# Kernel tuning notes

Measured on AMD Instinct MI355X. Metric: run time of the kernel, lower is better.

## Reference

```python
import jax, jax.numpy as jnp
import numpy as np

B, T, N, F, C, H, O = 4, 8, 4096, 32, 32, 64, 1
RADIUS = 50.0   # adjacency_threshold on pairwise distance
EPS = 1e-5      # batchnorm eps


def setup_inputs() -> dict:
    key = jax.random.key(0)
    ks = jax.random.split(key, 8)
    x = jax.random.normal(ks[0], (B, T, N, F), jnp.float32)
    # dist_mat from random 2D node locations in a 1000x1000 area; avg degree ~32
    loc = jax.random.uniform(ks[1], (N, 2), jnp.float32) * 1000.0
    d2 = jnp.sum((loc[:, None, :] - loc[None, :, :]) ** 2, axis=-1)  # [N,N]
    adj = (d2 < RADIUS ** 2).astype(jnp.float32)                     # includes self (d=0)
    dinv = 1.0 / jnp.sqrt(jnp.maximum(adj.sum(-1), 1.0))
    adj_norm = adj * dinv[:, None] * dinv[None, :]                   # D^-1/2 A D^-1/2
    s = 0.05
    return dict(
        x=x,
        adj_norm=adj_norm,
        bn_gamma=jnp.ones((F,), jnp.float32),
        bn_beta=jnp.zeros((F,), jnp.float32),
        W_gcn=jax.random.normal(ks[2], (F, C), jnp.float32) * s,
        b_gcn=jnp.zeros((C,), jnp.float32),
        W_ih=jax.random.normal(ks[3], (C, 3 * H), jnp.float32) * s,
        W_hh=jax.random.normal(ks[4], (H, 3 * H), jnp.float32) * s,
        b_ih=jnp.zeros((3 * H,), jnp.float32),
        b_hh=jnp.zeros((3 * H,), jnp.float32),
        W_dense=jax.random.normal(ks[5], (H, O), jnp.float32) * s,
        b_dense=jnp.zeros((O,), jnp.float32),
    )


def reference(x, adj_norm, bn_gamma, bn_beta, W_gcn, b_gcn, W_ih, W_hh, b_ih, b_hh, W_dense, b_dense):
    # BatchNorm2d over feature channel (training-mode batch stats, biased var)
    mean = x.mean(axis=(0, 1, 2))
    var = x.var(axis=(0, 1, 2))
    xn = (x - mean) * jax.lax.rsqrt(var + EPS) * bn_gamma + bn_beta  # [B,T,N,F]
    # GCN association (same math every timestep -> batch over T)
    ya = jnp.einsum('mn,btnf->btmf', adj_norm, xn)                   # neighbor aggregate
    y = jnp.einsum('btnf,fc->btnc', ya, W_gcn) + b_gcn               # [B,T,N,C]
    # precompute input-gate projections, then scan GRU cell over time
    gi = jnp.einsum('btnc,ch->btnh', y, W_ih) + b_ih                 # [B,T,N,3H]
    gi = jnp.transpose(gi, (1, 0, 2, 3))                             # [T,B,N,3H]

    def step(h, g):
        gh = h @ W_hh + b_hh
        r = jax.nn.sigmoid(g[..., :H] + gh[..., :H])
        z = jax.nn.sigmoid(g[..., H:2 * H] + gh[..., H:2 * H])
        n = jnp.tanh(g[..., 2 * H:] + r * gh[..., 2 * H:])
        h_new = (1.0 - z) * n + z * h
        return h_new, h_new

    h0 = jnp.zeros((B, N, H), x.dtype)
    _, hs = jax.lax.scan(step, h0, gi)                               # [T,B,N,H]
    out = jnp.transpose(hs, (1, 0, 2, 3)) @ W_dense + b_dense        # [B,T,N,O]
    return out
```

## Files before the change

### kernel.cpp

```cpp
#include <hip/hip_runtime.h>
#include <hip/hip_bf16.h>
#include <stdint.h>

#define B_ 4
#define T_ 8
#define N_ 4096
#define F_ 32
#define BT_ (B_*T_)
#define ROWS_ (B_*N_)
#define CAP_ 128
#define EPS_ 1e-5f
#define NELEM_ (B_*T_*N_*F_)

#define WS_BNP    0
#define WS_ROWSUM 16384
#define WS_DEG    (WS_ROWSUM + 4096)
#define WS_FRG    (WS_DEG + 4096)
#define WS_PAIR   (WS_FRG + 52*256)
#define WS_XA     (WS_PAIR + 4096*CAP_*2)

typedef float v4f __attribute__((ext_vector_type(4)));
typedef _Float16 half8 __attribute__((ext_vector_type(8)));
union HU { uint32_t u[4]; half8 v; };

__device__ inline float sigm_f(float x) {
  return __builtin_amdgcn_rcpf(1.0f + __expf(-x));
}
__device__ inline uint32_t f16pair(float a, float b) {
  union { _Float16 h; unsigned short s; } x, y;
  x.h = (_Float16)a; y.h = (_Float16)b;
  return (uint32_t)x.s | ((uint32_t)y.s << 16);
}
__device__ inline void sp2(float a0, float a1, uint32_t& hi, uint32_t& lo) {
  _Float16 h0 = (_Float16)a0, h1 = (_Float16)a1;
  float r0 = a0 - (float)h0, r1 = a1 - (float)h1;
  union { _Float16 h; unsigned short s; } u0, u1, v0, v1;
  u0.h = h0; u1.h = h1; v0.h = (_Float16)r0; v1.h = (_Float16)r1;
  hi = (uint32_t)u0.s | ((uint32_t)u1.s << 16);
  lo = (uint32_t)v0.s | ((uint32_t)v1.s << 16);
}

__global__ void __launch_bounds__(256)
k_pre(const float* __restrict__ x, const float* __restrict__ A, float* __restrict__ ws) {
  if (blockIdx.x < 2048) {
    int m0 = blockIdx.x * 2;
    __shared__ int cnt[2];
    __shared__ float wsum[4][2];
    if (threadIdx.x < 2) cnt[threadIdx.x] = 0;
    __syncthreads();
    int* deg = (int*)&ws[WS_DEG];
    float2* pair = (float2*)&ws[WS_PAIR];
    const float4* A4 = (const float4*)(A + (size_t)m0 * N_);
    float4 av4[8];
#pragma unroll
    for (int r = 0; r < 2; r++)
#pragma unroll
      for (int i = 0; i < 4; i++) av4[r * 4 + i] = A4[r * 1024 + threadIdx.x + 256 * i];
    float lsum[2] = {0.f, 0.f};
#pragma unroll
    for (int r = 0; r < 2; r++)
#pragma unroll
      for (int i = 0; i < 4; i++) {
        float av[4] = {av4[r*4+i].x, av4[r*4+i].y, av4[r*4+i].z, av4[r*4+i].w};
        int nb4 = (threadIdx.x + 256 * i) * 4;
#pragma unroll
        for (int e = 0; e < 4; e++) {
          float a = av[e];
          if (a != 0.0f) {
            int p = atomicAdd(&cnt[r], 1);
            if (p < CAP_) pair[(size_t)(m0 + r) * CAP_ + p] = make_float2(__int_as_float((nb4 + e) * F_), a);
            lsum[r] += a;
          }
        }
      }
#pragma unroll
    for (int r = 0; r < 2; r++) {
      float s = lsum[r];
#pragma unroll
      for (int off = 32; off > 0; off >>= 1) s += __shfl_xor(s, off, 64);
      if ((threadIdx.x & 63) == 0) wsum[threadIdx.x >> 6][r] = s;
    }
    __syncthreads();
#pragma unroll
    for (int r = 0; r < 2; r++) {
      int c = cnt[r];
      for (int p = c + threadIdx.x; p < 68; p += 256)
        pair[(size_t)(m0 + r) * CAP_ + p] = make_float2(__int_as_float(0), 0.0f);
    }
    if (threadIdx.x < 2) {
      int r = threadIdx.x;
      deg[m0 + r] = min(cnt[r], CAP_);
      ws[WS_ROWSUM + m0 + r] = wsum[0][r] + wsum[1][r] + wsum[2][r] + wsum[3][r];
    }
  } else {
    int bnb = blockIdx.x - 2048;
    const float4* x4 = (const float4*)x;
    int tid = bnb * 256 + threadIdx.x;
    float s[4] = {0,0,0,0}, s2[4] = {0,0,0,0};
    for (int i = tid; i < NELEM_ / 4; i += 256 * 256) {
      float4 v = x4[i];
      s[0] += v.x; s2[0] += v.x * v.x;
      s[1] += v.y; s2[1] += v.y * v.y;
      s[2] += v.z; s2[2] += v.z * v.z;
      s[3] += v.w; s2[3] += v.w * v.w;
    }
    __shared__ float ls[256][4], ls2[256][4];
#pragma unroll
    for (int r = 0; r < 4; r++) { ls[threadIdx.x][r] = s[r]; ls2[threadIdx.x][r] = s2[r]; }
    __syncthreads();
    int t = threadIdx.x;
    if (t < 32) {
      int g = t >> 2, r = t & 3;
      float a = 0.f;
      for (int q = g; q < 256; q += 8) a += ls[q][r];
      ws[WS_BNP + bnb * 64 + t] = a;
    } else if (t < 64) {
      int cch = t - 32;
      int g = cch >> 2, r = cch & 3;
      float b2 = 0.f;
      for (int q = g; q < 256; q += 8) b2 += ls2[q][r];
      ws[WS_BNP + bnb * 64 + t] = b2;
    }
  }
}

#define AGG_STEP(d) { \
    float vv = pv[d]; \
    v4f t0 = pb0[d], t1 = pb1[d], t2 = pb2[d], t3 = pb3[d]; \
    float2 p = pl[row * 69 + k + 4 + d]; \
    int off = __float_as_int(p.x) + fo; \
    pv[d] = p.y; \
    pb0[d] = *(const v4f*)(xb0 + off); \
    pb1[d] = *(const v4f*)(xb1 + off); \
    pb2[d] = *(const v4f*)(xb2 + off); \
    pb3[d] = *(const v4f*)(xb3 + off); \
    acc0 += vv * t0; acc1 += vv * t1; acc2 += vv * t2; acc3 += vv * t3; }

__global__ void __launch_bounds__(256, 4)
k_aggf(const float* __restrict__ x, const float* __restrict__ gamma,
       const float* __restrict__ beta, const float* __restrict__ Wg,
       const float* __restrict__ bg, const float* __restrict__ Wih,
       const float* __restrict__ bih, const float* __restrict__ Whh,
       const float* __restrict__ bhh, float* __restrict__ ws) {
  __shared__ float2 pl[32 * 69];
  int tid = threadIdx.x;
  if (blockIdx.x >= 1024) {
    float* fs   = (float*)pl;
    float* bnp4 = fs;
    float* bns  = fs + 256;
    float* scl  = fs + 320;
    float* shf  = fs + 352;
    float* ps   = fs + 384;
    float* Wg_s = fs + 416;
    float* Wic  = fs + 1440;
    float* Wxc  = fs + 1952;
    float* UsV  = fs + 2464;
    float* Whc  = fs + 2496;
    int fi = blockIdx.x - 1024;
    int mt, kt;
    if (fi < 32)      { mt = fi >> 2;              kt = fi & 3; }
    else if (fi < 40) { mt = 8 + ((fi - 32) >> 1); kt = (fi & 1) ? 3 : 0; }
    else              { int r = fi - 40; mt = 12 + r / 3; kt = 1 + r % 3; }
    int cls = mt >> 2;
    int colbase = (cls < 2) ? mt * 16 : 128 + (mt & 3) * 16;
    if (kt == 1 || kt == 2) {
      for (int e = tid; e < 512; e += 256) {
        int r = e >> 4, cc = e & 15;
        Whc[e] = Whh[(size_t)((kt - 1) * 32 + r) * 192 + colbase + cc];
      }
    } else {
      ((float4*)Wg_s)[tid] = ((const float4*)Wg)[tid];
      for (int e = tid; e < 512; e += 256) {
        int r = e >> 4, cc = e & 15;
        Wic[e] = Wih[(size_t)r * 192 + colbase + cc];
      }
      int g = tid >> 6, cch = tid & 63;
      float a = 0.f;
      for (int i = 0; i < 64; i++) a += ws[WS_BNP + (size_t)(g + 4 * i) * 64 + cch];
      bnp4[g * 64 + cch] = a;
    }
    __syncthreads();
    if ((kt == 0 || kt == 3) && tid < 64)
      bns[tid] = bnp4[tid] + bnp4[64 + tid] + bnp4[128 + tid] + bnp4[192 + tid];
    __syncthreads();
    if ((kt == 0 || kt == 3) && tid < 32) {
      float cntf = (float)(B_ * T_ * N_);
      float mean = bns[tid] / cntf;
      float var = bns[32 + tid] / cntf - mean * mean;
      float sc = gamma[tid] * rsqrtf(var + EPS_);
      scl[tid] = sc;
      shf[tid] = beta[tid] - mean * sc;
    }
    __syncthreads();
    if (kt == 3 && tid < 32) {
      float acc = 0.f;
#pragma unroll
      for (int f = 0; f < 32; f++) acc += shf[f] * Wg_s[f * 32 + tid];
      ps[tid] = acc;
    }
    __syncthreads();
    if (kt == 0) {
      for (int e = tid; e < 512; e += 256) {
        int f = e >> 4, cc = e & 15;
        float acc = 0.f;
#pragma unroll
        for (int m = 0; m < 32; m++) acc += Wg_s[f * 32 + m] * Wic[m * 16 + cc];
        Wxc[e] = scl[f] * acc;
      }
    } else if (kt == 3) {
      if (tid < 16) {
        float au = 0.f;
#pragma unroll
        for (int c2 = 0; c2 < 32; c2++) au += ps[c2] * Wic[c2 * 16 + tid];
        UsV[tid] = au;
      } else if (tid < 32) {
        int cc = tid - 16;
        float av = 0.f;
#pragma unroll
        for (int c2 = 0; c2 < 32; c2++) av += bg[c2] * Wic[c2 * 16 + cc];
        UsV[16 + cc] = av + bih[colbase + cc];
      }
    }
    __syncthreads();
    if (tid < 64) {
      int L = tid, q = L >> 4, c = L & 15;
      uint32_t* wsu = (uint32_t*)ws;
#pragma unroll
      for (int d = 0; d < 4; d++) {
        float a01[2];
#pragma unroll
        for (int h2 = 0; h2 < 2; h2++) {
          int kk = q * 8 + 2 * d + h2;
          float v;
          if (kt == 0)       v = Wxc[kk * 16 + c];
          else if (kt != 3)  v = Whc[kk * 16 + c];
          else if (kk == 0)  v = (cls == 3) ? 0.f : UsV[c];
          else if (kk == 1)  v = (cls < 2) ? (UsV[16 + c] + bhh[colbase + c])
                                           : (cls == 2 ? UsV[16 + c] : bhh[colbase + c]);
          else               v = 0.f;
          a01[h2] = v;
        }
        wsu[WS_FRG + fi * 256 + L * 4 + d] = f16pair(a01[0], a01[1]);
      }
    }
    return;
  }
  int bid2 = blockIdx.x;
  int chunk = bid2 & 7;
  int mg = bid2 >> 3;
  int row = tid >> 3, f4 = tid & 7;
  int m = mg * 32 + row;
  const int* deg = (const int*)&ws[WS_DEG];
  const float2* pair = (const float2*)&ws[WS_PAIR];
  for (int qq = tid; qq < 32 * 68; qq += 256) {
    int r = qq / 68, sl = qq - r * 68;
    pl[r * 69 + sl] = pair[(size_t)(mg * 32 + r) * CAP_ + sl];
  }
  __syncthreads();
  int d0 = deg[m];
  int dm = min(d0, 64);
  int bound = dm;
  bound = max(bound, __shfl_xor(bound, 8, 64));
  bound = max(bound, __shfl_xor(bound, 16, 64));
  bound = max(bound, __shfl_xor(bound, 32, 64));
  bound = (bound + 3) & ~3;
  int bt0 = chunk * 4;
  const float* xb0 = x + (size_t)bt0 * N_ * F_;
  const float* xb1 = xb0 + N_ * F_;
  const float* xb2 = xb0 + 2 * N_ * F_;
  const float* xb3 = xb0 + 3 * N_ * F_;
  int fo = f4 * 4;
  v4f acc0 = {0,0,0,0}, acc1 = {0,0,0,0}, acc2 = {0,0,0,0}, acc3 = {0,0,0,0};
  v4f pb0[4], pb1[4], pb2[4], pb3[4];
  float pv[4];
#pragma unroll
  for (int d = 0; d < 4; d++) {
    float2 p = pl[row * 69 + d];
    int off = __float_as_int(p.x) + fo;
    pv[d] = p.y;
    pb0[d] = *(const v4f*)(xb0 + off);
    pb1[d] = *(const v4f*)(xb1 + off);
    pb2[d] = *(const v4f*)(xb2 + off);
    pb3[d] = *(const v4f*)(xb3 + off);
  }
  for (int k = 0; k < bound; k += 4) {
    AGG_STEP(0) AGG_STEP(1) AGG_STEP(2) AGG_STEP(3)
  }
  if (d0 > 64) {
    for (int k = 64; k < d0; k++) {
      float2 p = pair[(size_t)m * CAP_ + k];
      int off = __float_as_int(p.x) + fo;
      float vv = p.y;
      acc0 += vv * *(const v4f*)(xb0 + off);
      acc1 += vv * *(const v4f*)(xb1 + off);
      acc2 += vv * *(const v4f*)(xb2 + off);
      acc3 += vv * *(const v4f*)(xb3 + off);
    }
  }
  size_t ob = (size_t)bt0 * N_ * F_ + m * F_ + fo;
  *(v4f*)(ws + WS_XA + ob) = acc0;
  *(v4f*)(ws + WS_XA + ob + (size_t)N_ * F_) = acc1;
  *(v4f*)(ws + WS_XA + ob + (size_t)2 * N_ * F_) = acc2;
  *(v4f*)(ws + WS_XA + ob + (size_t)3 * N_ * F_) = acc3;
}

#define LDA(fi) (*(const half8*)(frg + (fi)*256 + L*4))
#define DO1(A_, fi, BH, BL) { half8 af = LDA(fi); \
  A_ = __builtin_amdgcn_mfma_f32_16x16x32_f16(af, BH, A_, 0, 0, 0); \
  A_ = __builtin_amdgcn_mfma_f32_16x16x32_f16(af, BL, A_, 0, 0, 0); }
#define DO1C(A_, C_, fi, BH, BL) { half8 af = LDA(fi); \
  A_ = __builtin_amdgcn_mfma_f32_16x16x32_f16(af, BH, C_, 0, 0, 0); \
  A_ = __builtin_amdgcn_mfma_f32_16x16x32_f16(af, BL, A_, 0, 0, 0); }

__global__ void __launch_bounds__(256, 2)
k_gru(const float* __restrict__ Wd, const float* __restrict__ bd,
      const float* __restrict__ ws, float* __restrict__ out) {
  __shared__ uint32_t frg[52 * 256];
  __shared__ uint32_t hx[2 * 1344];
  __shared__ float obuf[2][16];
  {
    const uint4* gf = (const uint4*)(ws + WS_FRG);
    uint4* sf = (uint4*)frg;
    for (int i = threadIdx.x; i < 52 * 64; i += 256) sf[i] = gf[i];
  }
  __syncthreads();
  int wid = threadIdx.x >> 6, L = threadIdx.x & 63;
  int grp = wid >> 1, half = wid & 1, h2 = half * 2;
  int q = L >> 4, c = L & 15;
  uint32_t* hxg = hx + grp * 1344;
  int rg0 = blockIdx.x * 32 + grp * 16;
  int b = rg0 >> 12;
  int node0 = rg0 & (N_ - 1);
  int fR0 = 4 * h2, fR1 = 4 * h2 + 4;
  int fZ0 = 16 + 4 * h2, fZ1 = 20 + 4 * h2;
  int fN0 = 32 + 2 * h2, fN1 = 34 + 2 * h2;
  int fG0 = 40 + 3 * h2, fG1 = 43 + 3 * h2;
  float wdv[2][4];
#pragma unroll
  for (int lg = 0; lg < 2; lg++)
#pragma unroll
    for (int r = 0; r < 4; r++) wdv[lg][r] = Wd[16 * (h2 + lg) + 4 * q + r];
  float bdv = bd[0];

  HU b3h, b3l;
#pragma unroll
  for (int d = 0; d < 4; d++) { b3h.u[d] = 0; b3l.u[d] = 0; }
  {
    float rsv = ws[WS_ROWSUM + node0 + c];
    uint32_t rhi, rlo;
    sp2(rsv, 1.0f, rhi, rlo);
    if (q == 0) { b3h.u[0] = rhi; b3l.u[0] = rlo & 0xFFFFu; }
  }

  v4f bias[8];
  {
    v4f z4 = {0.f, 0.f, 0.f, 0.f};
    DO1C(bias[0], z4, fR0 + 3, b3h.v, b3l.v)
    DO1C(bias[1], z4, fR1 + 3, b3h.v, b3l.v)
    DO1C(bias[2], z4, fZ0 + 3, b3h.v, b3l.v)
    DO1C(bias[3], z4, fZ1 + 3, b3h.v, b3l.v)
    DO1C(bias[4], z4, fN0 + 1, b3h.v, b3l.v)
    DO1C(bias[5], z4, fN1 + 1, b3h.v, b3l.v)
    DO1C(bias[6], z4, fG0 + 2, b3h.v, b3l.v)
    DO1C(bias[7], z4, fG1 + 2, b3h.v, b3l.v)
  }

  float h[2][4];
#pragma unroll
  for (int lg = 0; lg < 2; lg++)
#pragma unroll
    for (int r = 0; r < 4; r++) h[lg][r] = 0.f;

  const float* xab = ws + WS_XA;
  size_t xo0 = ((size_t)(b * T_) * N_ + node0 + c) * F_ + q * 8;
  float4 curA = *(const float4*)(xab + xo0);
  float4 curB = *(const float4*)(xab + xo0 + 4);
  float4 nxA, nxB;

#pragma unroll 1
  for (int t = 0; t < T_; t++) {
    HU b1h, b1l, b2h, b2l;
    if (t > 0) {
#pragma unroll
      for (int d = 0; d < 4; d++) {
        b1h.u[d] = hxg[((4 * q + d) * 2 + 0) * 21 + c];
        b1l.u[d] = hxg[((4 * q + d) * 2 + 1) * 21 + c];
        b2h.u[d] = hxg[((16 + 4 * q + d) * 2 + 0) * 21 + c];
        b2l.u[d] = hxg[((16 + 4 * q + d) * 2 + 1) * 21 + c];
      }
    }
    __syncthreads();
    if (t < T_ - 1) {
      size_t xo = ((size_t)(b * T_ + t + 1) * N_ + node0 + c) * F_ + q * 8;
      nxA = *(const float4*)(xab + xo);
      nxB = *(const float4*)(xab + xo + 4);
    }
    HU b0h, b0l;
    sp2(curA.x, curA.y, b0h.u[0], b0l.u[0]);
    sp2(curA.z, curA.w, b0h.u[1], b0l.u[1]);
    sp2(curB.x, curB.y, b0h.u[2], b0l.u[2]);
    sp2(curB.z, curB.w, b0h.u[3], b0l.u[3]);
    v4f acc[8];
    if (t > 0) {
      DO1C(acc[0], bias[0], fR0 + 1, b1h.v, b1l.v)
      DO1C(acc[1], bias[1], fR1 + 1, b1h.v, b1l.v)
      DO1C(acc[2], bias[2], fZ0 + 1, b1h.v, b1l.v)
      DO1C(acc[3], bias[3], fZ1 + 1, b1h.v, b1l.v)
      DO1C(acc[6], bias[6], fG0,     b1h.v, b1l.v)
      DO1C(acc[7], bias[7], fG1,     b1h.v, b1l.v)
      DO1(acc[0], fR0 + 2, b2h.v, b2l.v)
      DO1(acc[1], fR1 + 2, b2h.v, b2l.v)
      DO1(acc[2], fZ0 + 2, b2h.v, b2l.v)
      DO1(acc[3], fZ1 + 2, b2h.v, b2l.v)
      DO1(acc[6], fG0 + 1, b2h.v, b2l.v)
      DO1(acc[7], fG1 + 1, b2h.v, b2l.v)
      DO1(acc[0], fR0, b0h.v, b0l.v)
      DO1(acc[1], fR1, b0h.v, b0l.v)
      DO1(acc[2], fZ0, b0h.v, b0l.v)
      DO1(acc[3], fZ1, b0h.v, b0l.v)
      DO1C(acc[4], bias[4], fN0, b0h.v, b0l.v)
      DO1C(acc[5], bias[5], fN1, b0h.v, b0l.v)
    } else {
      DO1C(acc[0], bias[0], fR0, b0h.v, b0l.v)
      DO1C(acc[1], bias[1], fR1, b0h.v, b0l.v)
      DO1C(acc[2], bias[2], fZ0, b0h.v, b0l.v)
      DO1C(acc[3], bias[3], fZ1, b0h.v, b0l.v)
      DO1C(acc[4], bias[4], fN0, b0h.v, b0l.v)
      DO1C(acc[5], bias[5], fN1, b0h.v, b0l.v)
      acc[6] = bias[6]; acc[7] = bias[7];
    }
    float o = 0.f;
#pragma unroll
    for (int lg = 0; lg < 2; lg++)
#pragma unroll
      for (int r = 0; r < 4; r++) {
        float rr = sigm_f(acc[lg][r]);
        float zz = sigm_f(acc[2 + lg][r]);
        float nn = 2.0f * sigm_f(2.0f * (acc[4 + lg][r] + rr * acc[6 + lg][r])) - 1.0f;
        float hn = zz * (h[lg][r] - nn) + nn;
        h[lg][r] = hn;
        o += wdv[lg][r] * hn;
      }
    o += __shfl_xor(o, 16, 64);
    o += __shfl_xor(o, 32, 64);
    if (half == 1 && L < 16) obuf[grp][L] = o;
    if (t < T_ - 1) {
#pragma unroll
      for (int lg = 0; lg < 2; lg++)
#pragma unroll
        for (int rp = 0; rp < 2; rp++) {
          uint32_t phi, plo;
          sp2(h[lg][2 * rp], h[lg][2 * rp + 1], phi, plo);
          int pidx = 8 * (h2 + lg) + 2 * q + rp;
          hxg[(pidx * 2 + 0) * 21 + c] = phi;
          hxg[(pidx * 2 + 1) * 21 + c] = plo;
        }
    }
    __syncthreads();
    if (half == 0 && L < 16)
      out[(size_t)(b * T_ + t) * N_ + node0 + L] = o + obuf[grp][L] + bdv;
    curA = nxA; curB = nxB;
  }
}

extern "C" void kernel_launch(void* const* d_in, const int* in_sizes, int n_in,
                              void* d_out, int out_size, void* d_ws, size_t ws_size,
                              hipStream_t stream) {
  const float* x     = (const float*)d_in[0];
  const float* adj   = (const float*)d_in[1];
  const float* gamma = (const float*)d_in[2];
  const float* beta  = (const float*)d_in[3];
  const float* Wg    = (const float*)d_in[4];
  const float* bg    = (const float*)d_in[5];
  const float* Wih   = (const float*)d_in[6];
  const float* Whh   = (const float*)d_in[7];
  const float* bih   = (const float*)d_in[8];
  const float* bhh   = (const float*)d_in[9];
  const float* Wd    = (const float*)d_in[10];
  const float* bd    = (const float*)d_in[11];
  float* ws = (float*)d_ws;
  float* out = (float*)d_out;

  k_pre<<<2048 + 256, 256, 0, stream>>>(x, adj, ws);
  k_aggf<<<1024 + 52, 256, 0, stream>>>(x, gamma, beta, Wg, bg, Wih, bih, Whh, bhh, ws);
  k_gru<<<512, 256, 0, stream>>>(Wd, bd, ws, out);
}
```

Measured before the change: 177.7 us.

## Gather fp16 copy of input in neighbor aggregation, remap threads to 2 timesteps

```diff
diff --git a/kernel.cpp b/kernel.cpp
--- a/kernel.cpp
+++ b/kernel.cpp
@@ -18,6 +18,7 @@
 #define WS_FRG    (WS_DEG + 4096)
 #define WS_PAIR   (WS_FRG + 52*256)
 #define WS_XA     (WS_PAIR + 4096*CAP_*2)
+#define WS_X16    (WS_XA + NELEM_)
 
 typedef float v4f __attribute__((ext_vector_type(4)));
 typedef _Float16 half8 __attribute__((ext_vector_type(8)));
@@ -95,6 +96,7 @@
   } else {
     int bnb = blockIdx.x - 2048;
     const float4* x4 = (const float4*)x;
+    uint2* x16 = (uint2*)(ws + WS_X16);
     int tid = bnb * 256 + threadIdx.x;
     float s[4] = {0,0,0,0}, s2[4] = {0,0,0,0};
     for (int i = tid; i < NELEM_ / 4; i += 256 * 256) {
@@ -103,6 +105,10 @@
       s[1] += v.y; s2[1] += v.y * v.y;
       s[2] += v.z; s2[2] += v.z * v.z;
       s[3] += v.w; s2[3] += v.w * v.w;
+      uint2 hp;
+      hp.x = f16pair(v.x, v.y);
+      hp.y = f16pair(v.z, v.w);
+      x16[i] = hp;
     }
     __shared__ float ls[256][4], ls2[256][4];
 #pragma unroll
@@ -126,15 +132,16 @@
 
 #define AGG_STEP(d) { \
     float vv = pv[d]; \
-    v4f t0 = pb0[d], t1 = pb1[d], t2 = pb2[d], t3 = pb3[d]; \
+    half8 t0 = pb0[d], t1 = pb1[d]; \
     float2 p = pl[row * 69 + k + 4 + d]; \
     int off = __float_as_int(p.x) + fo; \
     pv[d] = p.y; \
-    pb0[d] = *(const v4f*)(xb0 + off); \
-    pb1[d] = *(const v4f*)(xb1 + off); \
-    pb2[d] = *(const v4f*)(xb2 + off); \
-    pb3[d] = *(const v4f*)(xb3 + off); \
-    acc0 += vv * t0; acc1 += vv * t1; acc2 += vv * t2; acc3 += vv * t3; }
+    pb0[d] = *(const half8*)(xh0 + off); \
+    pb1[d] = *(const half8*)(xh1 + off); \
+    _Pragma("unroll") \
+    for (int j = 0; j < 8; j++) { \
+      acc0[j] += vv * (float)t0[j]; \
+      acc1[j] += vv * (float)t1[j]; } }
 
 __global__ void __launch_bounds__(256, 4)
 k_aggf(const float* __restrict__ x, const float* __restrict__ gamma,
@@ -248,7 +255,9 @@
   int bid2 = blockIdx.x;
   int chunk = bid2 & 7;
   int mg = bid2 >> 3;
-  int row = tid >> 3, f4 = tid & 7;
+  int row = (tid >> 2) & 31;
+  int f8 = tid & 3;
+  int sg = tid >> 7;
   int m = mg * 32 + row;
   const int* deg = (const int*)&ws[WS_DEG];
   const float2* pair = (const float2*)&ws[WS_PAIR];
@@ -260,28 +269,28 @@
   int d0 = deg[m];
   int dm = min(d0, 64);
   int bound = dm;
+  bound = max(bound, __shfl_xor(bound, 4, 64));
   bound = max(bound, __shfl_xor(bound, 8, 64));
   bound = max(bound, __shfl_xor(bound, 16, 64));
   bound = max(bound, __shfl_xor(bound, 32, 64));
   bound = (bound + 3) & ~3;
-  int bt0 = chunk * 4;
-  const float* xb0 = x + (size_t)bt0 * N_ * F_;
-  const float* xb1 = xb0 + N_ * F_;
-  const float* xb2 = xb0 + 2 * N_ * F_;
-  const float* xb3 = xb0 + 3 * N_ * F_;
-  int fo = f4 * 4;
-  v4f acc0 = {0,0,0,0}, acc1 = {0,0,0,0}, acc2 = {0,0,0,0}, acc3 = {0,0,0,0};
-  v4f pb0[4], pb1[4], pb2[4], pb3[4];
+  int bt0 = chunk * 4 + 2 * sg;
+  const _Float16* xg = (const _Float16*)(ws + WS_X16);
+  const _Float16* xh0 = xg + (size_t)bt0 * N_ * F_;
+  const _Float16* xh1 = xh0 + N_ * F_;
+  int fo = f8 * 8;
+  float acc0[8], acc1[8];
+#pragma unroll
+  for (int j = 0; j < 8; j++) { acc0[j] = 0.f; acc1[j] = 0.f; }
+  half8 pb0[4], pb1[4];
   float pv[4];
 #pragma unroll
   for (int d = 0; d < 4; d++) {
     float2 p = pl[row * 69 + d];
     int off = __float_as_int(p.x) + fo;
     pv[d] = p.y;
-    pb0[d] = *(const v4f*)(xb0 + off);
-    pb1[d] = *(const v4f*)(xb1 + off);
-    pb2[d] = *(const v4f*)(xb2 + off);
-    pb3[d] = *(const v4f*)(xb3 + off);
+    pb0[d] = *(const half8*)(xh0 + off);
+    pb1[d] = *(const half8*)(xh1 + off);
   }
   for (int k = 0; k < bound; k += 4) {
     AGG_STEP(0) AGG_STEP(1) AGG_STEP(2) AGG_STEP(3)
@@ -291,17 +300,22 @@
       float2 p = pair[(size_t)m * CAP_ + k];
       int off = __float_as_int(p.x) + fo;
       float vv = p.y;
-      acc0 += vv * *(const v4f*)(xb0 + off);
-      acc1 += vv * *(const v4f*)(xb1 + off);
-      acc2 += vv * *(const v4f*)(xb2 + off);
-      acc3 += vv * *(const v4f*)(xb3 + off);
+#pragma unroll
+      for (int j = 0; j < 8; j++) {
+        acc0[j] += vv * (float)xh0[off + j];
+        acc1[j] += vv * (float)xh1[off + j];
+      }
     }
   }
   size_t ob = (size_t)bt0 * N_ * F_ + m * F_ + fo;
-  *(v4f*)(ws + WS_XA + ob) = acc0;
-  *(v4f*)(ws + WS_XA + ob + (size_t)N_ * F_) = acc1;
-  *(v4f*)(ws + WS_XA + ob + (size_t)2 * N_ * F_) = acc2;
-  *(v4f*)(ws + WS_XA + ob + (size_t)3 * N_ * F_) = acc3;
+  v4f s0a = {acc0[0], acc0[1], acc0[2], acc0[3]};
+  v4f s0b = {acc0[4], acc0[5], acc0[6], acc0[7]};
+  v4f s1a = {acc1[0], acc1[1], acc1[2], acc1[3]};
+  v4f s1b = {acc1[4], acc1[5], acc1[6], acc1[7]};
+  *(v4f*)(ws + WS_XA + ob) = s0a;
+  *(v4f*)(ws + WS_XA + ob + 4) = s0b;
+  *(v4f*)(ws + WS_XA + ob + (size_t)N_ * F_) = s1a;
+  *(v4f*)(ws + WS_XA + ob + (size_t)N_ * F_ + 4) = s1b;
 }
 
 #define LDA(fi) (*(const half8*)(frg + (fi)*256 + L*4))
```

After: 176.8 us. No clear change (-0.5%).
